# Kernel optimization log

Hardware: AMD Instinct MI355X
Metric: run time of the kernel (lower is better)

Reference implementation:

```python
import jax, jax.numpy as jnp
import numpy as np
import math

EMB = 768
HEADS = 12
HEAD_DIM = EMB // HEADS
FF = 3072
EPS = 1e-5


def setup_inputs() -> dict:
    key = jax.random.key(0)
    ks = jax.random.split(key, 12)
    s = 0.02
    return {
        "x": jax.random.normal(ks[0], (8, 1024, EMB), dtype=jnp.float32),
        "qkv_w": jax.random.normal(ks[1], (EMB, 3 * EMB), dtype=jnp.float32) * s,
        "qkv_b": jnp.zeros((3 * EMB,), dtype=jnp.float32),
        "out_w": jax.random.normal(ks[2], (EMB, EMB), dtype=jnp.float32) * s,
        "out_b": jnp.zeros((EMB,), dtype=jnp.float32),
        "ln1_g": jnp.ones((EMB,), dtype=jnp.float32),
        "ln1_b": jnp.zeros((EMB,), dtype=jnp.float32),
        "ln2_g": jnp.ones((EMB,), dtype=jnp.float32),
        "ln2_b": jnp.zeros((EMB,), dtype=jnp.float32),
        "fc1_w": jax.random.normal(ks[3], (EMB, FF), dtype=jnp.float32) * s,
        "fc1_b": jnp.zeros((FF,), dtype=jnp.float32),
        "fc2_w": jax.random.normal(ks[4], (FF, EMB), dtype=jnp.float32) * s,
        "fc2_b": jnp.zeros((EMB,), dtype=jnp.float32),
    }


def layernorm(x, g, b):
    mu = jnp.mean(x, axis=-1, keepdims=True)
    var = jnp.var(x, axis=-1, keepdims=True)
    return (x - mu) * jax.lax.rsqrt(var + EPS) * g + b


def new_gelu(x):
    c = math.sqrt(2.0 / math.pi)
    return 0.5 * x * (1.0 + jnp.tanh(c * (x + 0.044715 * x * x * x)))


def reference(x, qkv_w, qkv_b, out_w, out_b, ln1_g, ln1_b, ln2_g, ln2_b,
              fc1_w, fc1_b, fc2_w, fc2_b):
    B, S, _ = x.shape
    # --- attention sublayer (pre-LN) ---
    h = layernorm(x, ln1_g, ln1_b)
    qkv = h @ qkv_w + qkv_b                      # [B,S,3E]
    q, k, v = jnp.split(qkv, 3, axis=-1)
    def heads(t):
        return t.reshape(B, S, HEADS, HEAD_DIM).transpose(0, 2, 1, 3)  # [B,H,S,D]
    q, k, v = heads(q), heads(k), heads(v)
    scores = jnp.einsum('bhsd,bhtd->bhst', q, k) / math.sqrt(HEAD_DIM)
    probs = jax.nn.softmax(scores, axis=-1)
    attn = jnp.einsum('bhst,bhtd->bhsd', probs, v)
    attn = attn.transpose(0, 2, 1, 3).reshape(B, S, EMB)
    attn = attn @ out_w + out_b
    x = x + attn
    # --- MLP sublayer (pre-LN) ---
    h = layernorm(x, ln2_g, ln2_b)
    h = new_gelu(h @ fc1_w + fc1_b)
    h = h @ fc2_w + fc2_b
    return x + h
```

## Files before the change

kernel.cpp:

```cpp
#include <hip/hip_runtime.h>

typedef __bf16 bf16x8 __attribute__((ext_vector_type(8)));
typedef __bf16 bf16x4 __attribute__((ext_vector_type(4)));
typedef __bf16 bf16x2 __attribute__((ext_vector_type(2)));
typedef float  f32x4  __attribute__((ext_vector_type(4)));
typedef float  f32x16 __attribute__((ext_vector_type(16)));
typedef unsigned int uintx4 __attribute__((ext_vector_type(4)));

#define EMB 768
#define HEADS 12
#define HD 64
#define FF 3072
#define SEQ 1024
#define BATCH 8
#define ROWS (BATCH*SEQ)
#define QKVSZ ((size_t)BATCH*HEADS*SEQ*HD)

__device__ __forceinline__ void gload16(const void* g, void* l) {
    __builtin_amdgcn_global_load_lds(
        (const __attribute__((address_space(1))) unsigned int*)g,
        (__attribute__((address_space(3))) unsigned int*)l,
        16, 0, 0);
}

__device__ __forceinline__ unsigned int pkbf16(float lo, float hi) {
    bf16x2 w = { (__bf16)lo, (__bf16)hi };
    return __builtin_bit_cast(unsigned int, w);
}

__global__ __launch_bounds__(256) void ln_kernel(const float* __restrict__ x,
        const float* __restrict__ g, const float* __restrict__ b,
        __bf16* __restrict__ out)
{
    int row = blockIdx.x;
    int tid = threadIdx.x;
    const float* xr = x + (size_t)row * EMB;
    float v0 = xr[tid], v1 = xr[tid + 256], v2 = xr[tid + 512];
    float s  = v0 + v1 + v2;
    float ss = v0*v0 + v1*v1 + v2*v2;
    #pragma unroll
    for (int off = 32; off >= 1; off >>= 1) {
        s  += __shfl_xor(s, off);
        ss += __shfl_xor(ss, off);
    }
    __shared__ float red[2][4];
    int wave = tid >> 6;
    if ((tid & 63) == 0) { red[0][wave] = s; red[1][wave] = ss; }
    __syncthreads();
    s  = red[0][0] + red[0][1] + red[0][2] + red[0][3];
    ss = red[1][0] + red[1][1] + red[1][2] + red[1][3];
    float mu  = s * (1.0f / EMB);
    float var = ss * (1.0f / EMB) - mu * mu;
    float inv = rsqrtf(var + 1e-5f);
    __bf16* orow = out + (size_t)row * EMB;
    orow[tid]       = (__bf16)((v0 - mu) * inv * g[tid]       + b[tid]);
    orow[tid + 256] = (__bf16)((v1 - mu) * inv * g[tid + 256] + b[tid + 256]);
    orow[tid + 512] = (__bf16)((v2 - mu) * inv * g[tid + 512] + b[tid + 512]);
}

__global__ __launch_bounds__(256) void transpose_convert(const float* __restrict__ W,
        __bf16* __restrict__ WT, int K, int N)
{
    __shared__ float t[32][33];
    int nb = blockIdx.x * 32, kb = blockIdx.y * 32;
    int tx = threadIdx.x, ty = threadIdx.y;
    #pragma unroll
    for (int i = 0; i < 32; i += 8)
        t[ty + i][tx] = W[(size_t)(kb + ty + i) * N + nb + tx];
    __syncthreads();
    #pragma unroll
    for (int i = 0; i < 32; i += 8)
        WT[(size_t)(nb + ty + i) * K + kb + tx] = (__bf16)t[tx][ty + i];
}

template<int EPI>
__global__ __launch_bounds__(256) void gemm_bt(
    const __bf16* __restrict__ A, const __bf16* __restrict__ BT,
    const float* __restrict__ bias, const float* __restrict__ resid,
    void* __restrict__ outp, int M, int N, int K)
{
    __shared__ __bf16 Al[128][32];
    __shared__ __bf16 Bl[128][32];
    int tid  = threadIdx.x;
    int lane = tid & 63, wave = tid >> 6;
    int wr = wave >> 1, wc = wave & 1;
    int lr = lane & 15, lg = lane >> 4;
    int bn = blockIdx.x * 128, bm = blockIdx.y * 128;

    int srow = wave * 16 + (lane >> 2);
    int scol = (lane & 3) * 8;
    const __bf16* Ag0 = A  + (size_t)(bm + srow) * K + scol;
    const __bf16* Ag1 = Ag0 + (size_t)64 * K;
    const __bf16* Bg0 = BT + (size_t)(bn + srow) * K + scol;
    const __bf16* Bg1 = Bg0 + (size_t)64 * K;
    __bf16* lA0 = &Al[wave * 16][0];
    __bf16* lA1 = &Al[64 + wave * 16][0];
    __bf16* lB0 = &Bl[wave * 16][0];
    __bf16* lB1 = &Bl[64 + wave * 16][0];

    f32x4 acc[4][4];
    #pragma unroll
    for (int i = 0; i < 4; i++)
        #pragma unroll
        for (int j = 0; j < 4; j++) acc[i][j] = (f32x4){0.f, 0.f, 0.f, 0.f};

    for (int k0 = 0; k0 < K; k0 += 32) {
        gload16(Ag0 + k0, lA0);
        gload16(Ag1 + k0, lA1);
        gload16(Bg0 + k0, lB0);
        gload16(Bg1 + k0, lB1);
        __syncthreads();
        bf16x8 af[4], bfr[4];
        #pragma unroll
        for (int mi = 0; mi < 4; mi++) af[mi]  = *(const bf16x8*)&Al[wr*64 + mi*16 + lr][lg*8];
        #pragma unroll
        for (int ni = 0; ni < 4; ni++) bfr[ni] = *(const bf16x8*)&Bl[wc*64 + ni*16 + lr][lg*8];
        #pragma unroll
        for (int mi = 0; mi < 4; mi++)
            #pragma unroll
            for (int ni = 0; ni < 4; ni++)
                acc[mi][ni] = __builtin_amdgcn_mfma_f32_16x16x32_bf16(af[mi], bfr[ni], acc[mi][ni], 0, 0, 0);
        __syncthreads();
    }

    #pragma unroll
    for (int mi = 0; mi < 4; mi++) {
        int row = bm + wr*64 + mi*16 + lg*4;
        #pragma unroll
        for (int ni = 0; ni < 4; ni++) {
            int col = bn + wc*64 + ni*16 + lr;
            float bv = bias[col];
            #pragma unroll
            for (int j = 0; j < 4; j++) {
                int r = row + j;
                float v = acc[mi][ni][j] + bv;
                if (EPI == 0) {
                    int which = col / 768;
                    int cc = col - which * 768;
                    int hh = cc >> 6, dd = cc & 63;
                    int bb = r >> 10, s = r & 1023;
                    if (which == 0) {
                        v *= 0.125f;
                        ((__bf16*)outp)[((((size_t)bb * HEADS + hh) << 10) + s) * HD + dd] = (__bf16)v;
                    } else if (which == 1) {
                        ((__bf16*)outp)[QKVSZ + ((((size_t)bb * HEADS + hh) << 10) + s) * HD + dd] = (__bf16)v;
                    } else {
                        ((__bf16*)resid)[(((size_t)bb * HEADS + hh) * HD + dd) * SEQ + s] = (__bf16)v;
                    }
                } else if (EPI == 1) {
                    ((float*)outp)[(size_t)r * N + col] = v + resid[(size_t)r * N + col];
                } else {
                    float u = 0.7978845608028654f * (v + 0.044715f * v * v * v);
                    float e = __expf(2.0f * u);
                    float th = 1.0f - 2.0f / (e + 1.0f);
                    ((__bf16*)outp)[(size_t)r * N + col] = (__bf16)(0.5f * v * (1.0f + th));
                }
            }
        }
    }
}

__device__ __forceinline__ void loadK(bf16x8 (&dst)[8], const __bf16* Kp, int t, int lq, int hi) {
    #pragma unroll
    for (int kb = 0; kb < 2; kb++)
        #pragma unroll
        for (int dc = 0; dc < 4; dc++)
            dst[kb*4+dc] = *(const bf16x8*)(Kp + (size_t)(t*64 + kb*32 + lq) * HD + dc*16 + hi*8);
}

__global__ __launch_bounds__(256) void attn_kernel(
    const __bf16* __restrict__ Q, const __bf16* __restrict__ Km,
    const __bf16* __restrict__ Vt, __bf16* __restrict__ Aout)
{
    int blk = blockIdx.x;
    int bh = blk >> 3, qblk = blk & 7;
    int bb = bh / HEADS, hh = bh % HEADS;
    const __bf16* Qp = Q  + (size_t)bh * SEQ * HD;
    const __bf16* Kp = Km + (size_t)bh * SEQ * HD;
    const __bf16* Vp = Vt + (size_t)bh * HD * SEQ;
    int lane = threadIdx.x & 63, wave = threadIdx.x >> 6;
    int lq = lane & 31, hi = lane >> 5;
    int q0 = qblk * 128 + wave * 32;

    bf16x8 qf[4];
    #pragma unroll
    for (int dc = 0; dc < 4; dc++)
        qf[dc] = *(const bf16x8*)(Qp + (size_t)(q0 + lq) * HD + dc*16 + hi*8);

    f32x16 o0, o1;
    #pragma unroll
    for (int i = 0; i < 16; i++) { o0[i] = 0.f; o1[i] = 0.f; }
    float m = -1e30f, l = 0.0f;

    bf16x8 kfA[8], kfB[8];
    loadK(kfA, Kp, 0, lq, hi);

#define ATTN_TILE(KF, KFN, T)                                                        \
    do {                                                                             \
              \
        bf16x8 vf[8];                                                                \
        _Pragma("unroll")                                                            \
        for (int nb = 0; nb < 2; nb++)                                               \
            _Pragma("unroll")                                                        \
            for (int ks = 0; ks < 4; ks++)                                           \
                vf[nb*4+ks] = *(const bf16x8*)(Vp + (size_t)(nb*32 + lq) * SEQ       \
                                               + (T)*64 + ks*16 + hi*8);             \
        f32x16 st0, st1;                                                             \
        _Pragma("unroll")                                                            \
        for (int i = 0; i < 16; i++) { st0[i] = 0.f; st1[i] = 0.f; }                 \
        _Pragma("unroll")                                                            \
        for (int dc = 0; dc < 4; dc++)                                               \
            st0 = __builtin_amdgcn_mfma_f32_32x32x16_bf16(KF[dc], qf[dc], st0, 0, 0, 0); \
        _Pragma("unroll")                                                            \
        for (int dc = 0; dc < 4; dc++)                                               \
            st1 = __builtin_amdgcn_mfma_f32_32x32x16_bf16(KF[4+dc], qf[dc], st1, 0, 0, 0); \
                                        \
        loadK(KFN, Kp, (T)+1, lq, hi);                                               \
        float pmax = st0[0];                                                         \
        _Pragma("unroll")                                                            \
        for (int i = 1; i < 16; i++) pmax = fmaxf(pmax, st0[i]);                     \
        _Pragma("unroll")                                                            \
        for (int i = 0; i < 16; i++) pmax = fmaxf(pmax, st1[i]);                     \
        pmax = fmaxf(pmax, __shfl_xor(pmax, 32));                                    \
        if (__any(pmax > m + 8.0f)) {                                                \
            float mn = fmaxf(m, pmax);                                               \
            float sc = __expf(m - mn);                                               \
            _Pragma("unroll")                                                        \
            for (int r = 0; r < 16; r++) {                                           \
                float scr = __shfl(sc, (r & 3) + 8*(r >> 2) + 4*hi);                 \
                o0[r] *= scr; o1[r] *= scr;                                          \
            }                                                                        \
            l *= sc; m = mn;                                                         \
        }                                                                            \
        float p[32];                                                                 \
        _Pragma("unroll")                                                            \
        for (int i = 0; i < 16; i++) { p[i] = __expf(st0[i] - m);                    \
                                       p[16+i] = __expf(st1[i] - m); }               \
        float ps = 0.f;                                                              \
        _Pragma("unroll")                                                            \
        for (int i = 0; i < 32; i++) ps += p[i];                                     \
        ps += __shfl_xor(ps, 32);                                                    \
        l += ps;                                                                     \
        _Pragma("unroll")                                                            \
        for (int ks = 0; ks < 4; ks++) {                                             \
            unsigned int pa_ = pkbf16(p[ks*8+0], p[ks*8+1]);                         \
            unsigned int pc_ = pkbf16(p[ks*8+2], p[ks*8+3]);                         \
            unsigned int pb_ = pkbf16(p[ks*8+4], p[ks*8+5]);                         \
            unsigned int pd_ = pkbf16(p[ks*8+6], p[ks*8+7]);                         \
            asm("v_permlane32_swap_b32 %0, %1" : "+v"(pb_), "+v"(pa_));              \
            asm("v_permlane32_swap_b32 %0, %1" : "+v"(pd_), "+v"(pc_));              \
            uintx4 w_ = { pa_, pc_, pb_, pd_ };                                      \
            bf16x8 paf = __builtin_bit_cast(bf16x8, w_);                             \
            o0 = __builtin_amdgcn_mfma_f32_32x32x16_bf16(paf, vf[ks],   o0, 0, 0, 0); \
            o1 = __builtin_amdgcn_mfma_f32_32x32x16_bf16(paf, vf[4+ks], o1, 0, 0, 0); \
        }                                                                            \
    } while (0)

    #pragma unroll 1
    for (int t = 0; t < 16; t += 2) {
        ATTN_TILE(kfA, kfB, t);
        ATTN_TILE(kfB, kfA, t + 1);
    }
#undef ATTN_TILE

    float linv = 1.0f / l;
    #pragma unroll
    for (int r = 0; r < 16; r++) {
        int crow = (r & 3) + 8*(r >> 2) + 4*hi;
        float sc = __shfl(linv, crow);
        int q = q0 + crow;
        __bf16* dst = Aout + ((size_t)bb * SEQ + q) * EMB + hh * HD + lq;
        dst[0]  = (__bf16)(o0[r] * sc);
        dst[32] = (__bf16)(o1[r] * sc);
    }
}

extern "C" void kernel_launch(void* const* d_in, const int* in_sizes, int n_in,
                              void* d_out, int out_size, void* d_ws, size_t ws_size,
                              hipStream_t stream) {
    const float* x      = (const float*)d_in[0];
    const float* qkv_w  = (const float*)d_in[1];
    const float* qkv_b  = (const float*)d_in[2];
    const float* out_w  = (const float*)d_in[3];
    const float* out_b  = (const float*)d_in[4];
    const float* ln1_g  = (const float*)d_in[5];
    const float* ln1_b  = (const float*)d_in[6];
    const float* ln2_g  = (const float*)d_in[7];
    const float* ln2_b  = (const float*)d_in[8];
    const float* fc1_w  = (const float*)d_in[9];
    const float* fc1_b  = (const float*)d_in[10];
    const float* fc2_w  = (const float*)d_in[11];
    const float* fc2_b  = (const float*)d_in[12];

    char* ws = (char*)d_ws;
    __bf16* wqkvT  = (__bf16*)(ws + 0);
    __bf16* woutT  = (__bf16*)(ws + 3538944);
    __bf16* wfc1T  = (__bf16*)(ws + 4718592);
    __bf16* wfc2T  = (__bf16*)(ws + 9437184);
    float*  x1     = (float*) (ws + 14155776);
    __bf16* vt     = (__bf16*)(ws + 14155776);
    __bf16* hbuf   = (__bf16*)(ws + 39321600);
    __bf16* qbuf   = (__bf16*)(ws + 51904512);
    __bf16* attn   = (__bf16*)(ws + 89653248);
    __bf16* fc1out = (__bf16*)(ws + 51904512);

    transpose_convert<<<dim3(2304/32, 768/32),  dim3(32,8), 0, stream>>>(qkv_w, wqkvT, 768, 2304);
    transpose_convert<<<dim3(768/32,  768/32),  dim3(32,8), 0, stream>>>(out_w, woutT, 768, 768);
    transpose_convert<<<dim3(3072/32, 768/32),  dim3(32,8), 0, stream>>>(fc1_w, wfc1T, 768, 3072);
    transpose_convert<<<dim3(768/32,  3072/32), dim3(32,8), 0, stream>>>(fc2_w, wfc2T, 3072, 768);

    ln_kernel<<<ROWS, 256, 0, stream>>>(x, ln1_g, ln1_b, hbuf);
    gemm_bt<0><<<dim3(2304/128, ROWS/128), 256, 0, stream>>>(hbuf, wqkvT, qkv_b, (const float*)vt, qbuf, ROWS, 2304, 768);
    attn_kernel<<<BATCH*HEADS*(SEQ/128), 256, 0, stream>>>(qbuf, qbuf + QKVSZ, vt, attn);
    gemm_bt<1><<<dim3(768/128, ROWS/128), 256, 0, stream>>>(attn, woutT, out_b, x, x1, ROWS, 768, 768);
    ln_kernel<<<ROWS, 256, 0, stream>>>(x1, ln2_g, ln2_b, hbuf);
    gemm_bt<2><<<dim3(3072/128, ROWS/128), 256, 0, stream>>>(hbuf, wfc1T, fc1_b, nullptr, fc1out, ROWS, 3072, 768);
    gemm_bt<1><<<dim3(768/128, ROWS/128), 256, 0, stream>>>(fc1out, wfc2T, fc2_b, x1, (float*)d_out, ROWS, 768, 3072);
}
```

Measured before the change: 468.7 us.

## Add 256x256 double-buffered swizzled GEMM for QKV/FC1 and exp2 softmax

```diff
diff --git a/kernel.cpp b/kernel.cpp
--- a/kernel.cpp
+++ b/kernel.cpp
@@ -15,6 +15,7 @@
 #define BATCH 8
 #define ROWS (BATCH*SEQ)
 #define QKVSZ ((size_t)BATCH*HEADS*SEQ*HD)
+#define LOG2E 1.44269504088896f
 
 __device__ __forceinline__ void gload16(const void* g, void* l) {
     __builtin_amdgcn_global_load_lds(
@@ -74,10 +75,127 @@
 }
 
 template<int EPI>
+__global__ __launch_bounds__(512) void gemm256(
+    const __bf16* __restrict__ A, const __bf16* __restrict__ BT,
+    const float* __restrict__ bias, __bf16* __restrict__ vtout,
+    void* __restrict__ outp, int M, int N, int K)
+{
+    extern __shared__ char lds[];
+    int tid = threadIdx.x;
+    int lane = tid & 63, wid = tid >> 6;
+    int wr = wid >> 2, wc = wid & 3;
+    int lr = lane & 15, lg = lane >> 4;
+
+    int nbx = gridDim.x;
+    int nwg = nbx * gridDim.y;
+    int orig = blockIdx.y * nbx + blockIdx.x;
+    int q8 = nwg >> 3, r8 = nwg & 7;
+    int xcd = orig & 7, rest = orig >> 3;
+    int swz = (xcd < r8 ? xcd * (q8 + 1) : r8 * (q8 + 1) + (xcd - r8) * q8) + rest;
+    int bm = (swz / nbx) * 256;
+    int bn = (swz % nbx) * 256;
+
+    int srow = tid >> 3;
+    int scolb = ((tid & 7) * 16) ^ ((srow & 7) << 4);
+    const char* Ag = (const char*)A  + ((size_t)(bm + srow) * K) * 2 + scolb;
+    const char* Bg = (const char*)BT + ((size_t)(bn + srow) * K) * 2 + scolb;
+    size_t issue_stride = (size_t)64 * K * 2;
+
+#define STAGE256(buf, k0)                                                   \
+    do {                                                                    \
+        const char* ag_ = Ag + (size_t)(k0) * 2;                            \
+        const char* bg_ = Bg + (size_t)(k0) * 2;                            \
+        char* la_ = lds + (buf) * 65536 + wid * 1024;                       \
+        char* lb_ = la_ + 32768;                                            \
+        _Pragma("unroll")                                                   \
+        for (int i_ = 0; i_ < 4; i_++)                                      \
+            gload16(ag_ + i_ * issue_stride, la_ + i_ * 8192);              \
+        _Pragma("unroll")                                                   \
+        for (int i_ = 0; i_ < 4; i_++)                                      \
+            gload16(bg_ + i_ * issue_stride, lb_ + i_ * 8192);              \
+    } while (0)
+
+    int sxor = (lr & 7) << 4;
+    int koff0 = (lg * 16) ^ sxor;
+    int koff1 = (64 + lg * 16) ^ sxor;
+    int abase = (wr * 128 + lr) * 128;
+    int bbase = 32768 + (wc * 64 + lr) * 128;
+
+    f32x4 acc[8][4];
+    #pragma unroll
+    for (int i = 0; i < 8; i++)
+        #pragma unroll
+        for (int j = 0; j < 4; j++) acc[i][j] = (f32x4){0.f, 0.f, 0.f, 0.f};
+
+    int NT = K >> 6;
+    STAGE256(0, 0);
+    __syncthreads();
+    int cur = 0;
+    for (int t = 0; t < NT; ++t) {
+        if (t + 1 < NT) STAGE256(cur ^ 1, (t + 1) * 64);
+        const char* base = lds + cur * 65536;
+        #pragma unroll
+        for (int ksub = 0; ksub < 2; ksub++) {
+            int ko = ksub ? koff1 : koff0;
+            bf16x8 af[8], bfr[4];
+            #pragma unroll
+            for (int mi = 0; mi < 8; mi++)
+                af[mi] = *(const bf16x8*)(base + abase + mi * 2048 + ko);
+            #pragma unroll
+            for (int ni = 0; ni < 4; ni++)
+                bfr[ni] = *(const bf16x8*)(base + bbase + ni * 2048 + ko);
+            __builtin_amdgcn_s_setprio(1);
+            #pragma unroll
+            for (int mi = 0; mi < 8; mi++)
+                #pragma unroll
+                for (int ni = 0; ni < 4; ni++)
+                    acc[mi][ni] = __builtin_amdgcn_mfma_f32_16x16x32_bf16(af[mi], bfr[ni], acc[mi][ni], 0, 0, 0);
+            __builtin_amdgcn_s_setprio(0);
+        }
+        __syncthreads();
+        cur ^= 1;
+    }
+#undef STAGE256
+
+    #pragma unroll
+    for (int mi = 0; mi < 8; mi++) {
+        int row = bm + wr * 128 + mi * 16 + lg * 4;
+        #pragma unroll
+        for (int ni = 0; ni < 4; ni++) {
+            int col = bn + wc * 64 + ni * 16 + lr;
+            float bv = bias[col];
+            #pragma unroll
+            for (int j = 0; j < 4; j++) {
+                int r = row + j;
+                float v = acc[mi][ni][j] + bv;
+                if (EPI == 0) {
+                    int which = col / 768;
+                    int cc = col - which * 768;
+                    int hh = cc >> 6, dd = cc & 63;
+                    int bb = r >> 10, s = r & 1023;
+                    if (which == 0) {
+                        v *= 0.125f * LOG2E;
+                        ((__bf16*)outp)[((((size_t)bb * HEADS + hh) << 10) + s) * HD + dd] = (__bf16)v;
+                    } else if (which == 1) {
+                        ((__bf16*)outp)[QKVSZ + ((((size_t)bb * HEADS + hh) << 10) + s) * HD + dd] = (__bf16)v;
+                    } else {
+                        vtout[(((size_t)bb * HEADS + hh) * HD + dd) * SEQ + s] = (__bf16)v;
+                    }
+                } else {
+                    float u = 0.7978845608028654f * (v + 0.044715f * v * v * v);
+                    float e = __expf(2.0f * u);
+                    float th = 1.0f - 2.0f / (e + 1.0f);
+                    ((__bf16*)outp)[(size_t)r * N + col] = (__bf16)(0.5f * v * (1.0f + th));
+                }
+            }
+        }
+    }
+}
+
 __global__ __launch_bounds__(256) void gemm_bt(
     const __bf16* __restrict__ A, const __bf16* __restrict__ BT,
     const float* __restrict__ bias, const float* __restrict__ resid,
-    void* __restrict__ outp, int M, int N, int K)
+    float* __restrict__ outp, int M, int N, int K)
 {
     __shared__ __bf16 Al[128][32];
     __shared__ __bf16 Bl[128][32];
@@ -133,28 +251,7 @@
             #pragma unroll
             for (int j = 0; j < 4; j++) {
                 int r = row + j;
-                float v = acc[mi][ni][j] + bv;
-                if (EPI == 0) {
-                    int which = col / 768;
-                    int cc = col - which * 768;
-                    int hh = cc >> 6, dd = cc & 63;
-                    int bb = r >> 10, s = r & 1023;
-                    if (which == 0) {
-                        v *= 0.125f;
-                        ((__bf16*)outp)[((((size_t)bb * HEADS + hh) << 10) + s) * HD + dd] = (__bf16)v;
-                    } else if (which == 1) {
-                        ((__bf16*)outp)[QKVSZ + ((((size_t)bb * HEADS + hh) << 10) + s) * HD + dd] = (__bf16)v;
-                    } else {
-                        ((__bf16*)resid)[(((size_t)bb * HEADS + hh) * HD + dd) * SEQ + s] = (__bf16)v;
-                    }
-                } else if (EPI == 1) {
-                    ((float*)outp)[(size_t)r * N + col] = v + resid[(size_t)r * N + col];
-                } else {
-                    float u = 0.7978845608028654f * (v + 0.044715f * v * v * v);
-                    float e = __expf(2.0f * u);
-                    float th = 1.0f - 2.0f / (e + 1.0f);
-                    ((__bf16*)outp)[(size_t)r * N + col] = (__bf16)(0.5f * v * (1.0f + th));
-                }
+                outp[(size_t)r * N + col] = acc[mi][ni][j] + bv + resid[(size_t)r * N + col];
             }
         }
     }
@@ -197,7 +294,6 @@
 
 #define ATTN_TILE(KF, KFN, T)                                                        \
     do {                                                                             \
-              \
         bf16x8 vf[8];                                                                \
         _Pragma("unroll")                                                            \
         for (int nb = 0; nb < 2; nb++)                                               \
@@ -214,7 +310,6 @@
         _Pragma("unroll")                                                            \
         for (int dc = 0; dc < 4; dc++)                                               \
             st1 = __builtin_amdgcn_mfma_f32_32x32x16_bf16(KF[4+dc], qf[dc], st1, 0, 0, 0); \
-                                        \
         loadK(KFN, Kp, (T)+1, lq, hi);                                               \
         float pmax = st0[0];                                                         \
         _Pragma("unroll")                                                            \
@@ -222,9 +317,9 @@
         _Pragma("unroll")                                                            \
         for (int i = 0; i < 16; i++) pmax = fmaxf(pmax, st1[i]);                     \
         pmax = fmaxf(pmax, __shfl_xor(pmax, 32));                                    \
-        if (__any(pmax > m + 8.0f)) {                                                \
+        if (__any(pmax > m + 11.5f)) {                                               \
             float mn = fmaxf(m, pmax);                                               \
-            float sc = __expf(m - mn);                                               \
+            float sc = exp2f(m - mn);                                                \
             _Pragma("unroll")                                                        \
             for (int r = 0; r < 16; r++) {                                           \
                 float scr = __shfl(sc, (r & 3) + 8*(r >> 2) + 4*hi);                 \
@@ -234,8 +329,8 @@
         }                                                                            \
         float p[32];                                                                 \
         _Pragma("unroll")                                                            \
-        for (int i = 0; i < 16; i++) { p[i] = __expf(st0[i] - m);                    \
-                                       p[16+i] = __expf(st1[i] - m); }               \
+        for (int i = 0; i < 16; i++) { p[i] = exp2f(st0[i] - m);                     \
+                                       p[16+i] = exp2f(st1[i] - m); }                \
         float ps = 0.f;                                                              \
         _Pragma("unroll")                                                            \
         for (int i = 0; i < 32; i++) ps += p[i];                                     \
@@ -304,16 +399,19 @@
     __bf16* attn   = (__bf16*)(ws + 89653248);
     __bf16* fc1out = (__bf16*)(ws + 51904512);
 
+    hipFuncSetAttribute((const void*)gemm256<0>, hipFuncAttributeMaxDynamicSharedMemorySize, 131072);
+    hipFuncSetAttribute((const void*)gemm256<2>, hipFuncAttributeMaxDynamicSharedMemorySize, 131072);
+
     transpose_convert<<<dim3(2304/32, 768/32),  dim3(32,8), 0, stream>>>(qkv_w, wqkvT, 768, 2304);
     transpose_convert<<<dim3(768/32,  768/32),  dim3(32,8), 0, stream>>>(out_w, woutT, 768, 768);
     transpose_convert<<<dim3(3072/32, 768/32),  dim3(32,8), 0, stream>>>(fc1_w, wfc1T, 768, 3072);
     transpose_convert<<<dim3(768/32,  3072/32), dim3(32,8), 0, stream>>>(fc2_w, wfc2T, 3072, 768);
 
     ln_kernel<<<ROWS, 256, 0, stream>>>(x, ln1_g, ln1_b, hbuf);
-    gemm_bt<0><<<dim3(2304/128, ROWS/128), 256, 0, stream>>>(hbuf, wqkvT, qkv_b, (const float*)vt, qbuf, ROWS, 2304, 768);
+    gemm256<0><<<dim3(2304/256, ROWS/256), 512, 131072, stream>>>(hbuf, wqkvT, qkv_b, vt, qbuf, ROWS, 2304, 768);
     attn_kernel<<<BATCH*HEADS*(SEQ/128), 256, 0, stream>>>(qbuf, qbuf + QKVSZ, vt, attn);
-    gemm_bt<1><<<dim3(768/128, ROWS/128), 256, 0, stream>>>(attn, woutT, out_b, x, x1, ROWS, 768, 768);
+    gemm_bt<<<dim3(768/128, ROWS/128), 256, 0, stream>>>(attn, woutT, out_b, x, x1, ROWS, 768, 768);
     ln_kernel<<<ROWS, 256, 0, stream>>>(x1, ln2_g, ln2_b, hbuf);
-    gemm_bt<2><<<dim3(3072/128, ROWS/128), 256, 0, stream>>>(hbuf, wfc1T, fc1_b, nullptr, fc1out, ROWS, 3072, 768);
-    gemm_bt<1><<<dim3(768/128, ROWS/128), 256, 0, stream>>>(fc1out, wfc2T, fc2_b, x1, (float*)d_out, ROWS, 768, 3072);
-}
+    gemm256<2><<<dim3(3072/256, ROWS/256), 512, 131072, stream>>>(hbuf, wfc1T, fc1_b, nullptr, fc1out, ROWS, 3072, 768);
+    gemm_bt<<<dim3(768/128, ROWS/128), 256, 0, stream>>>(fc1out, wfc2T, fc2_b, x1, (float*)d_out, ROWS, 768, 3072);
+}
```

New measurement: 474.7 us. About the same (+1.3%).

## Write V row-major from QKV GEMM, transpose separately, use exp2 softmax and XCD mapping

Applied to the files above, without the earlier changes.

```diff
diff --git a/kernel.cpp b/kernel.cpp
--- a/kernel.cpp
+++ b/kernel.cpp
@@ -15,6 +15,7 @@
 #define BATCH 8
 #define ROWS (BATCH*SEQ)
 #define QKVSZ ((size_t)BATCH*HEADS*SEQ*HD)
+#define LOG2E 1.44269504088896f
 
 __device__ __forceinline__ void gload16(const void* g, void* l) {
     __builtin_amdgcn_global_load_lds(
@@ -73,6 +74,28 @@
         WT[(size_t)(nb + ty + i) * K + kb + tx] = (__bf16)t[tx][ty + i];
 }
 
+__global__ __launch_bounds__(256) void vtrans_kernel(const __bf16* __restrict__ V,
+        __bf16* __restrict__ Vt)
+{
+    __shared__ __bf16 t[64][72];
+    int bh = blockIdx.x >> 4, st = blockIdx.x & 15;
+    const __bf16* Vp = V + ((size_t)bh * SEQ + st * 64) * HD;
+    int r  = threadIdx.x >> 3;
+    int c0 = (threadIdx.x & 7) * 8;
+    #pragma unroll
+    for (int rep = 0; rep < 2; rep++)
+        *(bf16x8*)&t[r + rep*32][c0] = *(const bf16x8*)(Vp + (size_t)(r + rep*32) * HD + c0);
+    __syncthreads();
+    #pragma unroll
+    for (int rep = 0; rep < 2; rep++) {
+        int dd = r + rep*32;
+        bf16x8 o;
+        #pragma unroll
+        for (int j = 0; j < 8; j++) o[j] = t[c0 + j][dd];
+        *(bf16x8*)(Vt + ((size_t)bh * HD + dd) * SEQ + st * 64 + c0) = o;
+    }
+}
+
 template<int EPI>
 __global__ __launch_bounds__(256) void gemm_bt(
     const __bf16* __restrict__ A, const __bf16* __restrict__ BT,
@@ -139,14 +162,9 @@
                     int cc = col - which * 768;
                     int hh = cc >> 6, dd = cc & 63;
                     int bb = r >> 10, s = r & 1023;
-                    if (which == 0) {
-                        v *= 0.125f;
-                        ((__bf16*)outp)[((((size_t)bb * HEADS + hh) << 10) + s) * HD + dd] = (__bf16)v;
-                    } else if (which == 1) {
-                        ((__bf16*)outp)[QKVSZ + ((((size_t)bb * HEADS + hh) << 10) + s) * HD + dd] = (__bf16)v;
-                    } else {
-                        ((__bf16*)resid)[(((size_t)bb * HEADS + hh) * HD + dd) * SEQ + s] = (__bf16)v;
-                    }
+                    if (which == 0) v *= 0.125f * LOG2E;
+                    ((__bf16*)outp)[(size_t)which * QKVSZ +
+                        ((((size_t)bb * HEADS + hh) << 10) + s) * HD + dd] = (__bf16)v;
                 } else if (EPI == 1) {
                     ((float*)outp)[(size_t)r * N + col] = v + resid[(size_t)r * N + col];
                 } else {
@@ -172,8 +190,10 @@
     const __bf16* __restrict__ Q, const __bf16* __restrict__ Km,
     const __bf16* __restrict__ Vt, __bf16* __restrict__ Aout)
 {
-    int blk = blockIdx.x;
-    int bh = blk >> 3, qblk = blk & 7;
+    int xcd  = blockIdx.x & 7;
+    int idx  = blockIdx.x >> 3;
+    int bh   = xcd * 12 + (idx % 12);
+    int qblk = idx / 12;
     int bb = bh / HEADS, hh = bh % HEADS;
     const __bf16* Qp = Q  + (size_t)bh * SEQ * HD;
     const __bf16* Kp = Km + (size_t)bh * SEQ * HD;
@@ -197,7 +217,6 @@
 
 #define ATTN_TILE(KF, KFN, T)                                                        \
     do {                                                                             \
-              \
         bf16x8 vf[8];                                                                \
         _Pragma("unroll")                                                            \
         for (int nb = 0; nb < 2; nb++)                                               \
@@ -214,7 +233,6 @@
         _Pragma("unroll")                                                            \
         for (int dc = 0; dc < 4; dc++)                                               \
             st1 = __builtin_amdgcn_mfma_f32_32x32x16_bf16(KF[4+dc], qf[dc], st1, 0, 0, 0); \
-                                        \
         loadK(KFN, Kp, (T)+1, lq, hi);                                               \
         float pmax = st0[0];                                                         \
         _Pragma("unroll")                                                            \
@@ -222,9 +240,9 @@
         _Pragma("unroll")                                                            \
         for (int i = 0; i < 16; i++) pmax = fmaxf(pmax, st1[i]);                     \
         pmax = fmaxf(pmax, __shfl_xor(pmax, 32));                                    \
-        if (__any(pmax > m + 8.0f)) {                                                \
+        if (__any(pmax > m + 11.5f)) {                                               \
             float mn = fmaxf(m, pmax);                                               \
-            float sc = __expf(m - mn);                                               \
+            float sc = exp2f(m - mn);                                                \
             _Pragma("unroll")                                                        \
             for (int r = 0; r < 16; r++) {                                           \
                 float scr = __shfl(sc, (r & 3) + 8*(r >> 2) + 4*hi);                 \
@@ -234,8 +252,8 @@
         }                                                                            \
         float p[32];                                                                 \
         _Pragma("unroll")                                                            \
-        for (int i = 0; i < 16; i++) { p[i] = __expf(st0[i] - m);                    \
-                                       p[16+i] = __expf(st1[i] - m); }               \
+        for (int i = 0; i < 16; i++) { p[i] = exp2f(st0[i] - m);                     \
+                                       p[16+i] = exp2f(st1[i] - m); }                \
         float ps = 0.f;                                                              \
         _Pragma("unroll")                                                            \
         for (int i = 0; i < 32; i++) ps += p[i];                                     \
@@ -310,7 +328,8 @@
     transpose_convert<<<dim3(768/32,  3072/32), dim3(32,8), 0, stream>>>(fc2_w, wfc2T, 3072, 768);
 
     ln_kernel<<<ROWS, 256, 0, stream>>>(x, ln1_g, ln1_b, hbuf);
-    gemm_bt<0><<<dim3(2304/128, ROWS/128), 256, 0, stream>>>(hbuf, wqkvT, qkv_b, (const float*)vt, qbuf, ROWS, 2304, 768);
+    gemm_bt<0><<<dim3(2304/128, ROWS/128), 256, 0, stream>>>(hbuf, wqkvT, qkv_b, nullptr, qbuf, ROWS, 2304, 768);
+    vtrans_kernel<<<BATCH*HEADS*(SEQ/64), 256, 0, stream>>>(qbuf + 2*QKVSZ, vt);
     attn_kernel<<<BATCH*HEADS*(SEQ/128), 256, 0, stream>>>(qbuf, qbuf + QKVSZ, vt, attn);
     gemm_bt<1><<<dim3(768/128, ROWS/128), 256, 0, stream>>>(attn, woutT, out_b, x, x1, ROWS, 768, 768);
     ln_kernel<<<ROWS, 256, 0, stream>>>(x1, ln2_g, ln2_b, hbuf);
```

Result: faster. 450.7 us (-3.8%).
